# Performance work log

Hardware: AMD Instinct MI355X
Metric: run time of the kernel (lower is better)

## Reference

```python
import jax, jax.numpy as jnp
import numpy as np

N_NODES = 20000
DIM = 128
N_EDGES = 500000
BATCH = 16384
EPS = 1e-6  # torch.nn.PairwiseDistance default eps


def setup_inputs() -> dict:
    key = jax.random.key(0)
    k = jax.random.split(key, 8)
    edges = jax.random.randint(k[0], (2, N_EDGES), 0, N_NODES, dtype=jnp.int64 if jax.config.jax_enable_x64 else jnp.int32)
    nodes_p_star = jnp.sort(jax.random.randint(k[1], (BATCH,), 0, N_NODES))
    nodes_p = jnp.sort(jax.random.randint(k[2], (BATCH,), 0, N_NODES))
    # learned parameters, init in [-1, 1) as in the torch module
    beta_p = 2.0 * jax.random.uniform(k[3], (N_NODES,), dtype=jnp.float32) - 1.0
    beta_p_star = 2.0 * jax.random.uniform(k[4], (N_NODES,), dtype=jnp.float32) - 1.0
    p = 2.0 * jax.random.uniform(k[5], (N_NODES, DIM), dtype=jnp.float32) - 1.0
    p_star = 2.0 * jax.random.uniform(k[6], (N_NODES, DIM), dtype=jnp.float32) - 1.0
    return {
        "edges": edges,
        "nodes_p_star": nodes_p_star,
        "nodes_p": nodes_p,
        "beta_p": beta_p,
        "beta_p_star": beta_p_star,
        "p": p,
        "p_star": p_star,
    }


def reference(edges, nodes_p_star, nodes_p, beta_p, beta_p_star, p, p_star):
    # ---- link term: sum over observed edges of (beta - dist) ----
    beta_pair = beta_p_star[edges[0]] + beta_p[edges[1]]  # [E]
    diff = p[edges[0]] - p_star[edges[1]]                 # [E, D]
    # torch PairwiseDistance adds eps to the difference before the norm
    z_dist = jnp.sqrt(jnp.sum((diff + EPS) ** 2, axis=-1))
    link_term = jnp.sum(beta_pair - z_dist)

    # ---- non-link term: triu-masked sum of exp(beta - cdist) ----
    bps = beta_p_star[nodes_p_star]   # [Ns]
    bp = beta_p[nodes_p]              # [Np]
    ps = p_star[nodes_p_star]         # [Ns, D]
    pp = p[nodes_p]                   # [Np, D]
    beta_mat = bps[None, :] + bp[:, None]          # [Np, Ns]
    # cdist(ps, pp) -> [Ns, Np] via Gram trick
    sq = (jnp.sum(ps * ps, axis=-1)[:, None]
          + jnp.sum(pp * pp, axis=-1)[None, :]
          - 2.0 * jnp.einsum('nd,md->nm', ps, pp))
    dist_mat = jnp.sqrt(jnp.maximum(sq, 0.0))      # [Ns, Np]
    intensity = jnp.exp(beta_mat.T - dist_mat)     # [Ns, Np]
    non_link = jnp.sum(jnp.triu(intensity, k=1))

    return -(link_term - non_link)
```

## Files before the change

### kernel.cpp

```cpp
#include <hip/hip_runtime.h>

#define N_NODES 20000
#define DIM 128
#define N_EDGES 500000
#define BATCH 16384
#define EPS 1e-6f
#define L2E 1.4426950408889634f

typedef _Float16 half8 __attribute__((ext_vector_type(8)));
typedef _Float16 half4_t __attribute__((ext_vector_type(4)));
typedef float f32x4 __attribute__((ext_vector_type(4)));
typedef float f32x2 __attribute__((ext_vector_type(2)));

__device__ __forceinline__ float fast_sqrtf(float x) {
#if __has_builtin(__builtin_amdgcn_sqrtf)
    return __builtin_amdgcn_sqrtf(x);
#else
    return sqrtf(x);
#endif
}
__device__ __forceinline__ float fast_exp2f(float x) {
#if __has_builtin(__builtin_amdgcn_exp2f)
    return __builtin_amdgcn_exp2f(x);
#else
    return exp2f(x);
#endif
}

#define NB_TILE 8256
#define NB_STEP 16512
#define N_BLK   512

#define OFF_PGEMM 0
#define OFF_CTR   16384
#define OFF_PSH   33280
#define OFF_PPH   4227584
#define OFF_N2S   8421888
#define OFF_N2P   8487424
#define OFF_BPS   8552960
#define OFF_BP    8618496
#define OFF_END   8684032

__global__ __launch_bounds__(256) void prep_kernel(
    const float* __restrict__ p, const float* __restrict__ p_star,
    const float* __restrict__ beta_p, const float* __restrict__ beta_ps,
    const int* __restrict__ nodes_ps, const int* __restrict__ nodes_p,
    _Float16* __restrict__ Ah, float* __restrict__ n2A, float* __restrict__ bA2,
    _Float16* __restrict__ Bh, float* __restrict__ n2B, float* __restrict__ bB2,
    unsigned* __restrict__ ctr)
{
    if (blockIdx.x == 0 && threadIdx.x == 0) *ctr = 0u;
    const int bx = blockIdx.x;
    const int g = threadIdx.x & 31;
    const int r8 = threadIdx.x >> 5;
    const bool isA = bx < 2048;
    const int row = (isA ? bx : bx - 2048) * 8 + r8;
    const int id = isA ? nodes_ps[row] : nodes_p[row];
    const float* src = isA ? p_star : p;
    float4 v = ((const float4*)(src + (size_t)id * DIM))[g];
    half4_t o;
    o[0] = (_Float16)v.x; o[1] = (_Float16)v.y; o[2] = (_Float16)v.z; o[3] = (_Float16)v.w;
    const int h = g >> 4;
    const int pc = ((g >> 1) & 7) ^ (row & 7);
    _Float16* dst = isA ? Ah : Bh;
    *(half4_t*)(dst + (size_t)row * DIM + (((h << 3) | pc) << 3) + (g & 1) * 4) = o;
    float nrm = v.x * v.x + v.y * v.y + v.z * v.z + v.w * v.w;
    #pragma unroll
    for (int m = 16; m >= 1; m >>= 1) nrm += __shfl_xor(nrm, m, 32);
    if (g == 0) {
        if (isA) { n2A[row] = nrm; bA2[row] = L2E * beta_ps[id]; }
        else     { n2B[row] = nrm; bB2[row] = L2E * beta_p[id]; }
    }
}

__device__ __forceinline__ void tile_of(int t, int& i0, int& tjb, bool& diag) {
    const int by = t / 129;
    const int bx = t - by * 129;
    const int len = 128 - by;
    int ti, tj;
    if (bx < len) { ti = by; tj = by + bx; }
    else          { ti = 127 - by; tj = 127 - (bx - len); }
    i0 = ti << 7; tjb = tj << 7; diag = (ti == tj);
}

#define STAGE_A(I0)                                                                \
    {                                                                              \
        _Pragma("unroll")                                                          \
        for (int u = 0; u < 4; ++u) {                                              \
            const int g8 = u * 8 + w;                                   \
            const int h = g8 >> 4, rg = g8 & 15;                                   \
            __builtin_amdgcn_global_load_lds(                                      \
                (const __attribute__((address_space(1))) void*)(gA +               \
                    (((size_t)((I0) + rg * 8 + (lane >> 3))) << 8)                 \
                    + (h << 7) + ((lane & 7) << 4)),                               \
                (__attribute__((address_space(3))) void*)(lds                      \
                    + h * 16384 + rg * 1024), 16, 0, 0);                           \
        }                                                                          \
    }

#define STAGE_B(JB)                                                                \
    {                                                                              \
        _Pragma("unroll")                                                          \
        for (int u = 0; u < 2; ++u) {                                              \
            const int g8 = u * 8 + w;                                   \
            const int h = g8 >> 3, rg = g8 & 7;                                    \
            __builtin_amdgcn_global_load_lds(                                      \
                (const __attribute__((address_space(1))) void*)(gB +               \
                    (((size_t)((JB) + rg * 8 + (lane >> 3))) << 8)                 \
                    + (h << 7) + ((lane & 7) << 4)),                               \
                (__attribute__((address_space(3))) void*)(lds + 32768              \
                    + h * 8192 + rg * 1024), 16, 0, 0);                            \
        }                                                                          \
    }

__global__ __launch_bounds__(512, 6) void main_kernel(
    const _Float16* __restrict__ Ag, const _Float16* __restrict__ Bg,
    const float* __restrict__ n2A, const float* __restrict__ n2B,
    const float* __restrict__ bA2, const float* __restrict__ bB2,
    const int* __restrict__ edges,
    const float* __restrict__ beta_p, const float* __restrict__ beta_ps,
    const float* __restrict__ pf, const float* __restrict__ psf,
    float* __restrict__ pgemm, unsigned* __restrict__ ctr,
    float* __restrict__ out)
{
    __shared__ __align__(16) _Float16 sm16[24576];
    __shared__ float smr[8];
    __shared__ int lastflag;

    const int b = blockIdx.x;
    const int tid = threadIdx.x;
    const int lane = tid & 63;
    const int w = tid >> 6;
    const int wm = w & 3;
    const int wn = w >> 2;
    const int quad = lane >> 4;
    const int lr = lane & 15;
    const int k7 = lr & 7;

    auto* lds = (__attribute__((address_space(3))) char*)sm16;
    const auto* gA = (const __attribute__((address_space(1))) char*)Ag;
    const auto* gB = (const __attribute__((address_space(1))) char*)Bg;

    float lsum = 0.f;
    f32x2 lacc = {0.f, 0.f};

    const int start = b * 32 + (b < 128 ? b : 128);
    const int tend = start + 32 + (b < 128 ? 1 : 0);

    int s = start;
    int i0, tjb; bool diag;
    {
        tile_of(s >> 1, i0, tjb, diag);
        const int hb = s & 1;
        STAGE_A(i0)
        STAGE_B(tjb + hb * 64)
    }
    __syncthreads();

    for (;;) {
        const int hb = s & 1;
        int cls = 0;
        if (diag) { const int cj = hb * 2 + wn; cls = (cj > wm) ? 0 : (cj == wm ? 1 : 2); }

        f32x4 acc[2][2] = {};
        if (cls != 2) {
            #pragma unroll
            for (int ks = 0; ks < 4; ++ks) {
                const int h = ks >> 1;
                const int pc = (((ks & 1) << 2) | quad) ^ k7;
                half8 af[2], bf[2];
                #pragma unroll
                for (int u = 0; u < 2; ++u)
                    af[u] = *(const half8*)&sm16[h * 8192 + (wm * 32 + u * 16 + lr) * 64 + pc * 8];
                #pragma unroll
                for (int v = 0; v < 2; ++v)
                    bf[v] = *(const half8*)&sm16[16384 + h * 4096 + (wn * 32 + v * 16 + lr) * 64 + pc * 8];
                #pragma unroll
                for (int mi = 0; mi < 2; ++mi)
                    #pragma unroll
                    for (int ni = 0; ni < 2; ++ni)
                        acc[mi][ni] = __builtin_amdgcn_mfma_f32_16x16x32_f16(
                            af[mi], bf[ni], acc[mi][ni], 0, 0, 0);
            }
        }

        const int ilo = i0 + wm * 32;
        const int jlo = tjb + hb * 64 + wn * 32;
        const int scur = s;
        __syncthreads();

        s += 1;
        const bool more = (s < tend);
        if (more) {
            const int pi0 = i0;
            tile_of(s >> 1, i0, tjb, diag);
            if (i0 != pi0) STAGE_A(i0)
            STAGE_B(tjb + (s & 1) * 64)
        }

        #pragma unroll
        for (int tt = 0; tt < 1; ++tt) {
            int e = scur * 32 + w * 4 + quad;
            if (e < N_EDGES) {
                int e0 = edges[e];
                int e1 = edges[N_EDGES + e];
                const float* ar = pf + (size_t)e0 * DIM + lr * 8;
                const float* br = psf + (size_t)e1 * DIM + lr * 8;
                f32x4 a0 = *(const f32x4*)ar;   f32x4 a1 = *(const f32x4*)(ar + 4);
                f32x4 b0 = *(const f32x4*)br;   f32x4 b1 = *(const f32x4*)(br + 4);
                float eb2 = (lr == 0) ? (beta_ps[e0] + beta_p[e1]) : 0.f;
                float ssum = 0.f;
                #pragma unroll
                for (int k = 0; k < 4; ++k) { float d = a0[k] - b0[k] + EPS; ssum = fmaf(d, d, ssum); }
                #pragma unroll
                for (int k = 0; k < 4; ++k) { float d = a1[k] - b1[k] + EPS; ssum = fmaf(d, d, ssum); }
                #pragma unroll
                for (int m = 8; m >= 1; m >>= 1) ssum += __shfl_xor(ssum, m, 16);
                if (lr == 0) lsum -= eb2 - fast_sqrtf(ssum);
            }
        }

        if (cls != 2) {
            f32x4 n2i[2], bi[2];
            #pragma unroll
            for (int mi = 0; mi < 2; ++mi) {
                n2i[mi] = *(const f32x4*)&n2A[ilo + mi * 16 + quad * 4];
                bi[mi]  = *(const f32x4*)&bA2[ilo + mi * 16 + quad * 4];
            }
            float n2j[2], bj[2];
            #pragma unroll
            for (int ni = 0; ni < 2; ++ni) {
                n2j[ni] = n2B[jlo + ni * 16 + lr];
                bj[ni]  = bB2[jlo + ni * 16 + lr];
            }

            #pragma unroll
            for (int mi = 0; mi < 2; ++mi)
                #pragma unroll
                for (int ni = 0; ni < 2; ++ni) {
                    const f32x4 d = acc[mi][ni];
                    #pragma unroll
                    for (int pr = 0; pr < 2; ++pr) {
                        f32x2 d2 = { d[2 * pr], d[2 * pr + 1] };
                        f32x2 t2 = { n2i[mi][2 * pr] + n2j[ni], n2i[mi][2 * pr + 1] + n2j[ni] };
                        f32x2 sq2 = d2 * -2.0f + t2;
                        f32x2 z2 = { 0.f, 0.f };
                        f32x2 mx2 = __builtin_elementwise_max(sq2, z2);
                        float s0 = fast_sqrtf(mx2[0]);
                        float s1 = fast_sqrtf(mx2[1]);
                        f32x2 bs2 = { bi[mi][2 * pr] + bj[ni], bi[mi][2 * pr + 1] + bj[ni] };
                        f32x2 sr2 = { s0, s1 };
                        f32x2 ar2 = sr2 * -L2E + bs2;
                        float e0 = fast_exp2f(ar2[0]);
                        float e1 = fast_exp2f(ar2[1]);
                        if (cls == 0) {
                            f32x2 e2 = { e0, e1 };
                            lacc += e2;
                        } else {
                            const int ig0 = ilo + mi * 16 + quad * 4 + 2 * pr;
                            const int jg = jlo + ni * 16 + lr;
                            if (jg > ig0)     lacc[0] += e0;
                            if (jg > ig0 + 1) lacc[1] += e1;
                        }
                    }
                }
        }

        if (!more) break;
        __syncthreads();
    }

    lsum += lacc[0] + lacc[1];
    #pragma unroll
    for (int m = 32; m >= 1; m >>= 1) lsum += __shfl_xor(lsum, m, 64);
    if (lane == 0) smr[w] = lsum;
    __syncthreads();
    if (tid == 0) {
        float ssum = 0.f;
        #pragma unroll
        for (int i = 0; i < 8; ++i) ssum += smr[i];
        pgemm[b] = ssum;
        unsigned prev = __hip_atomic_fetch_add(ctr, 1u, __ATOMIC_ACQ_REL,
                                               __HIP_MEMORY_SCOPE_AGENT);
        lastflag = (prev == N_BLK - 1) ? 1 : 0;
    }
    __syncthreads();

    if (lastflag) {
        float v = __hip_atomic_load(&pgemm[tid], __ATOMIC_RELAXED,
                                    __HIP_MEMORY_SCOPE_AGENT);
        #pragma unroll
        for (int m = 32; m >= 1; m >>= 1) v += __shfl_xor(v, m, 64);
        if (lane == 0) smr[w] = v;
        __syncthreads();
        if (tid == 0) {
            float tsum = 0.f;
            #pragma unroll
            for (int i = 0; i < 8; ++i) tsum += smr[i];
            out[0] = tsum;
        }
    }
}

extern "C" void kernel_launch(void* const* d_in, const int* in_sizes, int n_in,
                              void* d_out, int out_size, void* d_ws, size_t ws_size,
                              hipStream_t stream) {
    const int* edges = (const int*)d_in[0];
    const int* nodes_p_star = (const int*)d_in[1];
    const int* nodes_p = (const int*)d_in[2];
    const float* beta_p = (const float*)d_in[3];
    const float* beta_p_star = (const float*)d_in[4];
    const float* p = (const float*)d_in[5];
    const float* p_star = (const float*)d_in[6];

    char* ws = (char*)d_ws;
    float* pgemm = (float*)(ws + OFF_PGEMM);
    unsigned* ctr = (unsigned*)(ws + OFF_CTR);
    _Float16* psh = (_Float16*)(ws + OFF_PSH);
    _Float16* pph = (_Float16*)(ws + OFF_PPH);
    float* n2s = (float*)(ws + OFF_N2S);
    float* n2p = (float*)(ws + OFF_N2P);
    float* bps2 = (float*)(ws + OFF_BPS);
    float* bp2 = (float*)(ws + OFF_BP);

    prep_kernel<<<4096, 256, 0, stream>>>(
        p, p_star, beta_p, beta_p_star, nodes_p_star, nodes_p,
        psh, n2s, bps2, pph, n2p, bp2, ctr);

    main_kernel<<<N_BLK, 512, 0, stream>>>(
        psh, pph, n2s, n2p, bps2, bp2,
        edges, beta_p, beta_p_star, p, p_star,
        pgemm, ctr, (float*)d_out);
}
```

Baseline: 208.4 us.

## Process full 128x128 triangular tiles per step with 1024-thread blocks

```diff
diff --git a/kernel.cpp b/kernel.cpp
--- a/kernel.cpp
+++ b/kernel.cpp
@@ -28,7 +28,6 @@
 }
 
 #define NB_TILE 8256
-#define NB_STEP 16512
 #define N_BLK   512
 
 #define OFF_PGEMM 0
@@ -73,47 +72,35 @@
     }
 }
 
-__device__ __forceinline__ void tile_of(int t, int& i0, int& tjb, bool& diag) {
+__device__ __forceinline__ void tile_of(int t, int& i0, int& j0, bool& diag) {
     const int by = t / 129;
     const int bx = t - by * 129;
     const int len = 128 - by;
     int ti, tj;
     if (bx < len) { ti = by; tj = by + bx; }
     else          { ti = 127 - by; tj = 127 - (bx - len); }
-    i0 = ti << 7; tjb = tj << 7; diag = (ti == tj);
-}
-
-#define STAGE_A(I0)                                                                \
-    {                                                                              \
-        _Pragma("unroll")                                                          \
-        for (int u = 0; u < 4; ++u) {                                              \
-            const int g8 = u * 8 + w;                                   \
-            const int h = g8 >> 4, rg = g8 & 15;                                   \
-            __builtin_amdgcn_global_load_lds(                                      \
-                (const __attribute__((address_space(1))) void*)(gA +               \
-                    (((size_t)((I0) + rg * 8 + (lane >> 3))) << 8)                 \
-                    + (h << 7) + ((lane & 7) << 4)),                               \
-                (__attribute__((address_space(3))) void*)(lds                      \
-                    + h * 16384 + rg * 1024), 16, 0, 0);                           \
-        }                                                                          \
-    }
-
-#define STAGE_B(JB)                                                                \
+    i0 = ti << 7; j0 = tj << 7; diag = (ti == tj);
+}
+
+#define STAGE_ARR(BASE0, GSRC, LOFF)                                               \
     {                                                                              \
         _Pragma("unroll")                                                          \
         for (int u = 0; u < 2; ++u) {                                              \
-            const int g8 = u * 8 + w;                                   \
-            const int h = g8 >> 3, rg = g8 & 7;                                    \
+            const int g8 = u * 16 + w;                                  \
+            const int h = g8 >> 4, rg = g8 & 15;                                   \
             __builtin_amdgcn_global_load_lds(                                      \
-                (const __attribute__((address_space(1))) void*)(gB +               \
-                    (((size_t)((JB) + rg * 8 + (lane >> 3))) << 8)                 \
+                (const __attribute__((address_space(1))) void*)((GSRC) +           \
+                    (((size_t)((BASE0) + rg * 8 + (lane >> 3))) << 8)              \
                     + (h << 7) + ((lane & 7) << 4)),                               \
-                (__attribute__((address_space(3))) void*)(lds + 32768              \
-                    + h * 8192 + rg * 1024), 16, 0, 0);                            \
+                (__attribute__((address_space(3))) void*)(lds + (LOFF)             \
+                    + h * 16384 + rg * 1024), 16, 0, 0);                           \
         }                                                                          \
     }
 
-__global__ __launch_bounds__(512, 6) void main_kernel(
+#define STAGE_A(I0) STAGE_ARR(I0, gA, 0)
+#define STAGE_B(J0) STAGE_ARR(J0, gB, 32768)
+
+__global__ __launch_bounds__(1024, 8) void main_kernel(
     const _Float16* __restrict__ Ag, const _Float16* __restrict__ Bg,
     const float* __restrict__ n2A, const float* __restrict__ n2B,
     const float* __restrict__ bA2, const float* __restrict__ bB2,
@@ -123,8 +110,8 @@
     float* __restrict__ pgemm, unsigned* __restrict__ ctr,
     float* __restrict__ out)
 {
-    __shared__ __align__(16) _Float16 sm16[24576];
-    __shared__ float smr[8];
+    __shared__ __align__(16) _Float16 sm16[32768];
+    __shared__ float smr[16];
     __shared__ int lastflag;
 
     const int b = blockIdx.x;
@@ -144,23 +131,19 @@
     float lsum = 0.f;
     f32x2 lacc = {0.f, 0.f};
 
-    const int start = b * 32 + (b < 128 ? b : 128);
-    const int tend = start + 32 + (b < 128 ? 1 : 0);
-
-    int s = start;
-    int i0, tjb; bool diag;
-    {
-        tile_of(s >> 1, i0, tjb, diag);
-        const int hb = s & 1;
-        STAGE_A(i0)
-        STAGE_B(tjb + hb * 64)
-    }
+    const int start = b * 16 + (b < 64 ? b : 64);
+    const int tend = start + 16 + (b < 64 ? 1 : 0);
+
+    int t = start;
+    int i0, j0; bool diag;
+    tile_of(t, i0, j0, diag);
+    STAGE_A(i0)
+    STAGE_B(j0)
     __syncthreads();
 
     for (;;) {
-        const int hb = s & 1;
         int cls = 0;
-        if (diag) { const int cj = hb * 2 + wn; cls = (cj > wm) ? 0 : (cj == wm ? 1 : 2); }
+        if (diag) cls = (wn > wm) ? 0 : (wn == wm ? 1 : 2);
 
         f32x4 acc[2][2] = {};
         if (cls != 2) {
@@ -174,7 +157,7 @@
                     af[u] = *(const half8*)&sm16[h * 8192 + (wm * 32 + u * 16 + lr) * 64 + pc * 8];
                 #pragma unroll
                 for (int v = 0; v < 2; ++v)
-                    bf[v] = *(const half8*)&sm16[16384 + h * 4096 + (wn * 32 + v * 16 + lr) * 64 + pc * 8];
+                    bf[v] = *(const half8*)&sm16[16384 + h * 8192 + (wn * 32 + v * 16 + lr) * 64 + pc * 8];
                 #pragma unroll
                 for (int mi = 0; mi < 2; ++mi)
                     #pragma unroll
@@ -185,22 +168,21 @@
         }
 
         const int ilo = i0 + wm * 32;
-        const int jlo = tjb + hb * 64 + wn * 32;
-        const int scur = s;
+        const int jlo = j0 + wn * 32;
+        const int tcur = t;
         __syncthreads();
 
-        s += 1;
-        const bool more = (s < tend);
+        t += 1;
+        const bool more = (t < tend);
         if (more) {
             const int pi0 = i0;
-            tile_of(s >> 1, i0, tjb, diag);
+            tile_of(t, i0, j0, diag);
             if (i0 != pi0) STAGE_A(i0)
-            STAGE_B(tjb + (s & 1) * 64)
-        }
-
-        #pragma unroll
-        for (int tt = 0; tt < 1; ++tt) {
-            int e = scur * 32 + w * 4 + quad;
+            STAGE_B(j0)
+        }
+
+        {
+            int e = tcur * 64 + w * 4 + quad;
             if (e < N_EDGES) {
                 int e0 = edges[e];
                 int e1 = edges[N_EDGES + e];
@@ -278,7 +260,7 @@
     if (tid == 0) {
         float ssum = 0.f;
         #pragma unroll
-        for (int i = 0; i < 8; ++i) ssum += smr[i];
+        for (int i = 0; i < 16; ++i) ssum += smr[i];
         pgemm[b] = ssum;
         unsigned prev = __hip_atomic_fetch_add(ctr, 1u, __ATOMIC_ACQ_REL,
                                                __HIP_MEMORY_SCOPE_AGENT);
@@ -287,8 +269,10 @@
     __syncthreads();
 
     if (lastflag) {
-        float v = __hip_atomic_load(&pgemm[tid], __ATOMIC_RELAXED,
-                                    __HIP_MEMORY_SCOPE_AGENT);
+        float v = 0.f;
+        if (tid < N_BLK)
+            v = __hip_atomic_load(&pgemm[tid], __ATOMIC_RELAXED,
+                                  __HIP_MEMORY_SCOPE_AGENT);
         #pragma unroll
         for (int m = 32; m >= 1; m >>= 1) v += __shfl_xor(v, m, 64);
         if (lane == 0) smr[w] = v;
@@ -296,7 +280,7 @@
         if (tid == 0) {
             float tsum = 0.f;
             #pragma unroll
-            for (int i = 0; i < 8; ++i) tsum += smr[i];
+            for (int i = 0; i < 16; ++i) tsum += smr[i];
             out[0] = tsum;
         }
     }
@@ -327,7 +311,7 @@
         p, p_star, beta_p, beta_p_star, nodes_p_star, nodes_p,
         psh, n2s, bps2, pph, n2p, bp2, ctr);
 
-    main_kernel<<<N_BLK, 512, 0, stream>>>(
+    main_kernel<<<N_BLK, 1024, 0, stream>>>(
         psh, pph, n2s, n2p, bps2, bp2,
         edges, beta_p, beta_p_star, p, p_star,
         pgemm, ctr, (float*)d_out);
```

Result: no change. 205.0 us (-1.6%).

## Double-buffer B tile in LDS, prefetch edge loads, and remap block-to-run order

Applied to the files above, without the earlier changes.

```diff
diff --git a/kernel.cpp b/kernel.cpp
--- a/kernel.cpp
+++ b/kernel.cpp
@@ -98,7 +98,7 @@
         }                                                                          \
     }
 
-#define STAGE_B(JB)                                                                \
+#define STAGE_B(JB, BUFOFF)                                                        \
     {                                                                              \
         _Pragma("unroll")                                                          \
         for (int u = 0; u < 2; ++u) {                                              \
@@ -108,7 +108,7 @@
                 (const __attribute__((address_space(1))) void*)(gB +               \
                     (((size_t)((JB) + rg * 8 + (lane >> 3))) << 8)                 \
                     + (h << 7) + ((lane & 7) << 4)),                               \
-                (__attribute__((address_space(3))) void*)(lds + 32768              \
+                (__attribute__((address_space(3))) void*)(lds + 32768 + (BUFOFF)   \
                     + h * 8192 + rg * 1024), 16, 0, 0);                            \
         }                                                                          \
     }
@@ -123,7 +123,7 @@
     float* __restrict__ pgemm, unsigned* __restrict__ ctr,
     float* __restrict__ out)
 {
-    __shared__ __align__(16) _Float16 sm16[24576];
+    __shared__ __align__(16) _Float16 sm16[32768];
     __shared__ float smr[8];
     __shared__ int lastflag;
 
@@ -144,21 +144,44 @@
     float lsum = 0.f;
     f32x2 lacc = {0.f, 0.f};
 
-    const int start = b * 32 + (b < 128 ? b : 128);
-    const int tend = start + 32 + (b < 128 ? 1 : 0);
+    const int run = (b & 7) * 64 + (b >> 3);
+    const int start = run * 32 + (run < 128 ? run : 128);
+    const int tend = start + 32 + (run < 128 ? 1 : 0);
 
     int s = start;
     int i0, tjb; bool diag;
-    {
-        tile_of(s >> 1, i0, tjb, diag);
-        const int hb = s & 1;
-        STAGE_A(i0)
-        STAGE_B(tjb + hb * 64)
-    }
+    tile_of(s >> 1, i0, tjb, diag);
+    int cur = 0;
+    STAGE_A(i0)
+    STAGE_B(tjb + (s & 1) * 64, 0)
     __syncthreads();
 
     for (;;) {
         const int hb = s & 1;
+
+        const bool more = (s + 1 < tend);
+        int ni0 = i0, ntjb = tjb; bool ndiag = diag;
+        bool achg = false;
+        if (more) {
+            tile_of((s + 1) >> 1, ni0, ntjb, ndiag);
+            achg = (ni0 != i0);
+            if (!achg) STAGE_B(ntjb + ((s + 1) & 1) * 64, (cur ^ 1) * 16384)
+        }
+
+        const int e = s * 32 + w * 4 + quad;
+        const bool ev = (e < N_EDGES);
+        f32x4 la0 = {}, la1 = {}, lb0 = {}, lb1 = {};
+        float eb2 = 0.f;
+        if (ev) {
+            int e0 = edges[e];
+            int e1 = edges[N_EDGES + e];
+            const float* ar = pf + (size_t)e0 * DIM + lr * 8;
+            const float* br = psf + (size_t)e1 * DIM + lr * 8;
+            la0 = *(const f32x4*)ar;  la1 = *(const f32x4*)(ar + 4);
+            lb0 = *(const f32x4*)br;  lb1 = *(const f32x4*)(br + 4);
+            if (lr == 0) eb2 = beta_ps[e0] + beta_p[e1];
+        }
+
         int cls = 0;
         if (diag) { const int cj = hb * 2 + wn; cls = (cj > wm) ? 0 : (cj == wm ? 1 : 2); }
 
@@ -174,7 +197,7 @@
                     af[u] = *(const half8*)&sm16[h * 8192 + (wm * 32 + u * 16 + lr) * 64 + pc * 8];
                 #pragma unroll
                 for (int v = 0; v < 2; ++v)
-                    bf[v] = *(const half8*)&sm16[16384 + h * 4096 + (wn * 32 + v * 16 + lr) * 64 + pc * 8];
+                    bf[v] = *(const half8*)&sm16[16384 + cur * 8192 + h * 4096 + (wn * 32 + v * 16 + lr) * 64 + pc * 8];
                 #pragma unroll
                 for (int mi = 0; mi < 2; ++mi)
                     #pragma unroll
@@ -184,43 +207,20 @@
             }
         }
 
-        const int ilo = i0 + wm * 32;
-        const int jlo = tjb + hb * 64 + wn * 32;
-        const int scur = s;
-        __syncthreads();
-
-        s += 1;
-        const bool more = (s < tend);
-        if (more) {
-            const int pi0 = i0;
-            tile_of(s >> 1, i0, tjb, diag);
-            if (i0 != pi0) STAGE_A(i0)
-            STAGE_B(tjb + (s & 1) * 64)
-        }
-
-        #pragma unroll
-        for (int tt = 0; tt < 1; ++tt) {
-            int e = scur * 32 + w * 4 + quad;
-            if (e < N_EDGES) {
-                int e0 = edges[e];
-                int e1 = edges[N_EDGES + e];
-                const float* ar = pf + (size_t)e0 * DIM + lr * 8;
-                const float* br = psf + (size_t)e1 * DIM + lr * 8;
-                f32x4 a0 = *(const f32x4*)ar;   f32x4 a1 = *(const f32x4*)(ar + 4);
-                f32x4 b0 = *(const f32x4*)br;   f32x4 b1 = *(const f32x4*)(br + 4);
-                float eb2 = (lr == 0) ? (beta_ps[e0] + beta_p[e1]) : 0.f;
-                float ssum = 0.f;
-                #pragma unroll
-                for (int k = 0; k < 4; ++k) { float d = a0[k] - b0[k] + EPS; ssum = fmaf(d, d, ssum); }
-                #pragma unroll
-                for (int k = 0; k < 4; ++k) { float d = a1[k] - b1[k] + EPS; ssum = fmaf(d, d, ssum); }
-                #pragma unroll
-                for (int m = 8; m >= 1; m >>= 1) ssum += __shfl_xor(ssum, m, 16);
-                if (lr == 0) lsum -= eb2 - fast_sqrtf(ssum);
-            }
+        if (ev) {
+            float ssum = 0.f;
+            #pragma unroll
+            for (int k = 0; k < 4; ++k) { float d = la0[k] - lb0[k] + EPS; ssum = fmaf(d, d, ssum); }
+            #pragma unroll
+            for (int k = 0; k < 4; ++k) { float d = la1[k] - lb1[k] + EPS; ssum = fmaf(d, d, ssum); }
+            #pragma unroll
+            for (int m = 8; m >= 1; m >>= 1) ssum += __shfl_xor(ssum, m, 16);
+            if (lr == 0) lsum -= eb2 - fast_sqrtf(ssum);
         }
 
         if (cls != 2) {
+            const int ilo = i0 + wm * 32;
+            const int jlo = tjb + hb * 64 + wn * 32;
             f32x4 n2i[2], bi[2];
             #pragma unroll
             for (int mi = 0; mi < 2; ++mi) {
@@ -267,7 +267,13 @@
         }
 
         if (!more) break;
+        if (achg) {
+            __syncthreads();
+            STAGE_A(ni0)
+            STAGE_B(ntjb + ((s + 1) & 1) * 64, (cur ^ 1) * 16384)
+        }
         __syncthreads();
+        s += 1; i0 = ni0; tjb = ntjb; diag = ndiag; cur ^= 1;
     }
 
     lsum += lacc[0] + lacc[1];
```

New measurement: 214.6 us. 1.03x slower.
